# Kernel optimization log

Measured on AMD Instinct MI355X. Metric: run time of the kernel, lower is better.

Reference implementation:

```python
import jax, jax.numpy as jnp
import numpy as np

N, E = 50000, 800000
IN, HID, OUT = 128, 128, 64
BN_EPS = 1e-5


def _w(key, fan_in, fan_out):
    return jax.random.normal(key, (fan_in, fan_out), dtype=jnp.float32) / np.sqrt(fan_in)


def setup_inputs() -> dict:
    key = jax.random.key(0)
    ks = jax.random.split(key, 12)
    x = jax.random.normal(ks[0], (N, IN), dtype=jnp.float32)
    src = jax.random.randint(ks[1], (E,), 0, N, dtype=jnp.int32)
    dst = jax.random.randint(ks[2], (E,), 0, N, dtype=jnp.int32)
    eps = jax.random.normal(ks[3], (N, OUT), dtype=jnp.float32)
    return {
        "x": x, "src": src, "dst": dst, "eps": eps,
        # SAGEConv 1: in -> hidden (lin_l has bias, lin_r no bias, mean aggr)
        "W1l": _w(ks[4], IN, HID), "W1r": _w(ks[5], IN, HID), "b1": jnp.zeros((HID,), jnp.float32),
        "g1": jnp.ones((HID,), jnp.float32), "be1": jnp.zeros((HID,), jnp.float32),
        # SAGEConv 2: hidden -> 2*hidden
        "W2l": _w(ks[6], HID, 2 * HID), "W2r": _w(ks[7], HID, 2 * HID), "b2": jnp.zeros((2 * HID,), jnp.float32),
        "g2": jnp.ones((2 * HID,), jnp.float32), "be2": jnp.zeros((2 * HID,), jnp.float32),
        # SAGEConv 3: 2*hidden -> 2*out
        "W3l": _w(ks[8], 2 * HID, 2 * OUT), "W3r": _w(ks[9], 2 * HID, 2 * OUT), "b3": jnp.zeros((2 * OUT,), jnp.float32),
    }


def _sage(h, src, dst, Wl, Wr, b):
    # mean-aggregate source features at destination nodes, then two GEMMs
    msg = jax.ops.segment_sum(h[src], dst, num_segments=N)          # [N, F]
    deg = jax.ops.segment_sum(jnp.ones((src.shape[0],), h.dtype), dst, num_segments=N)
    aggr = msg / jnp.maximum(deg, 1.0)[:, None]
    return aggr @ Wl + h @ Wr + b


def _bn(h, gamma, beta):
    m = jnp.mean(h, axis=0)
    v = jnp.var(h, axis=0)
    return gamma * (h - m) * jax.lax.rsqrt(v + BN_EPS) + beta


def reference(x, src, dst, eps, W1l, W1r, b1, g1, be1, W2l, W2r, b2, g2, be2, W3l, W3r, b3):
    h = jax.nn.relu(_sage(x, src, dst, W1l, W1r, b1))
    h = _bn(h, g1, be1)                       # dropout = identity (eval)
    h = jax.nn.relu(_sage(h, src, dst, W2l, W2r, b2))
    h = _bn(h, g2, be2)
    h = _sage(h, src, dst, W3l, W3r, b3)      # [N, 2*OUT]
    mean, log_std = jnp.split(h, 2, axis=-1)
    z = mean + jnp.exp(log_std) * eps         # reparameterize
    return z
```

## Files before the change

kernel.cpp:

```cpp
#include <hip/hip_runtime.h>
#include <math.h>

#define N_NODES 50000
#define N_EDGES 800000
#define BN_EPS_F 1e-5f
#define SCAN_BS 512
#define SCAN_NB 98
#define GXP 392

typedef unsigned short ushort_t;
typedef unsigned int uint_t;
typedef __attribute__((ext_vector_type(8))) short bf16x8;
typedef __attribute__((ext_vector_type(4))) float f32x4;

static __device__ __forceinline__ float4 ld4(const float* p) {
    return *reinterpret_cast<const float4*>(p);
}
static __device__ __forceinline__ float bf2f(ushort_t u) {
    return __uint_as_float(((uint_t)u) << 16);
}
static __device__ __forceinline__ ushort_t f2b(float f) {
    uint_t u = __float_as_uint(f);
    u += 0x7fffu + ((u >> 16) & 1u);
    return (ushort_t)(u >> 16);
}
static __device__ __forceinline__ void gload16(const void* g, void* l) {
    __builtin_amdgcn_global_load_lds(
        (const __attribute__((address_space(1))) void*)g,
        (__attribute__((address_space(3))) void*)l, 16, 0, 0);
}


__global__ void k_zero_i32(int* __restrict__ p, int n) {
    int i = blockIdx.x * blockDim.x + threadIdx.x;
    if (i < n) p[i] = 0;
}

__global__ void k_countrank(const int* __restrict__ dst, int* __restrict__ deg,
                            int* __restrict__ rank) {
    int e = blockIdx.x * blockDim.x + threadIdx.x;
    if (e < N_EDGES) rank[e] = atomicAdd(&deg[dst[e]], 1);
}

__global__ void k_scan1(const int* __restrict__ deg, int* __restrict__ offs, int* __restrict__ bsum) {
    __shared__ int sh[SCAN_BS];
    int t = threadIdx.x;
    int g = blockIdx.x * SCAN_BS + t;
    int v = (g < N_NODES) ? deg[g] : 0;
    sh[t] = v;
    __syncthreads();
    for (int off = 1; off < SCAN_BS; off <<= 1) {
        int add = (t >= off) ? sh[t - off] : 0;
        __syncthreads();
        sh[t] += add;
        __syncthreads();
    }
    if (g < N_NODES) offs[g] = sh[t] - v;
    if (t == SCAN_BS - 1) bsum[blockIdx.x] = sh[t];
}

__global__ void k_scan2(int* __restrict__ bsum, int nb) {
    __shared__ int sh[128];
    int t = threadIdx.x;
    int v = (t < nb) ? bsum[t] : 0;
    sh[t] = v;
    __syncthreads();
    for (int off = 1; off < 128; off <<= 1) {
        int add = (t >= off) ? sh[t - off] : 0;
        __syncthreads();
        sh[t] += add;
        __syncthreads();
    }
    if (t < nb) bsum[t] = sh[t] - v;
}

__global__ void k_scan3(const int* __restrict__ deg, int* __restrict__ offs,
                        const int* __restrict__ bsum, float* __restrict__ inv_deg) {
    int g = blockIdx.x * blockDim.x + threadIdx.x;
    if (g < N_NODES) {
        offs[g] += bsum[g / SCAN_BS];
        int d = deg[g];
        inv_deg[g] = 1.0f / (float)(d > 1 ? d : 1);
    }
}

__global__ void k_fill2(const int* __restrict__ src, const int* __restrict__ dst,
                        const int* __restrict__ offs, const int* __restrict__ rank,
                        int* __restrict__ eids) {
    int e = blockIdx.x * blockDim.x + threadIdx.x;
    if (e < N_EDGES) eids[offs[dst[e]] + rank[e]] = src[e];
}


__global__ void k_f2b8(const float* __restrict__ in, ushort_t* __restrict__ out, int n8) {
    int i = blockIdx.x * blockDim.x + threadIdx.x;
    if (i >= n8) return;
    float4 a = ld4(in + (size_t)i * 8);
    float4 b = ld4(in + (size_t)i * 8 + 4);
    uint_t o0 = (uint_t)f2b(a.x) | ((uint_t)f2b(a.y) << 16);
    uint_t o1 = (uint_t)f2b(a.z) | ((uint_t)f2b(a.w) << 16);
    uint_t o2 = (uint_t)f2b(b.x) | ((uint_t)f2b(b.y) << 16);
    uint_t o3 = (uint_t)f2b(b.z) | ((uint_t)f2b(b.w) << 16);
    *reinterpret_cast<uint4*>(out + (size_t)i * 8) = make_uint4(o0, o1, o2, o3);
}

__global__ void k_prep1(const float* __restrict__ W1l, const float* __restrict__ W1r,
                        const float* __restrict__ W2l, ushort_t* __restrict__ wt1l,
                        ushort_t* __restrict__ wt1r, ushort_t* __restrict__ wt2l) {
    int idx = blockIdx.x * 256 + threadIdx.x;
    if (idx < 16384) {
        int f = idx >> 7, k = idx & 127;
        wt1l[idx] = f2b(W1l[(size_t)k * 128 + f]);
    } else if (idx < 32768) {
        int j = idx - 16384;
        int f = j >> 7, k = j & 127;
        wt1r[j] = f2b(W1r[(size_t)k * 128 + f]);
    } else {
        int j = idx - 32768;
        int f = j >> 7, k = j & 127;
        wt2l[j] = f2b(W2l[(size_t)k * 256 + f]);
    }
}

__global__ void k_prep2(const float* __restrict__ W2r, const float* __restrict__ b2,
                        const float* __restrict__ scsh1, ushort_t* __restrict__ wt2r,
                        float* __restrict__ bias2) {
    int bid = blockIdx.x;
    if (bid < 128) {
        int idx = bid * 256 + threadIdx.x;
        int f = idx >> 7, k = idx & 127;
        wt2r[idx] = f2b(scsh1[k] * W2r[(size_t)k * 256 + f]);
    } else {
        int f = threadIdx.x;
        float s = b2[f];
        for (int k = 0; k < 128; ++k) s += scsh1[128 + k] * W2r[(size_t)k * 256 + f];
        bias2[f] = s;
    }
}

__global__ void k_prep3(const float* __restrict__ W3l, const float* __restrict__ W3r,
                        const float* __restrict__ b3, const float* __restrict__ scsh2,
                        ushort_t* __restrict__ wt3l, ushort_t* __restrict__ wt3r,
                        float* __restrict__ bias3l, float* __restrict__ bias3r) {
    int bid = blockIdx.x;
    if (bid < 256) {
        int half = bid >> 7;
        int idx = (bid & 127) * 256 + threadIdx.x;
        int f = idx >> 8, k = idx & 255;
        const float* W = half ? W3r : W3l;
        ushort_t* WT = half ? wt3r : wt3l;
        WT[idx] = f2b(scsh2[k] * W[(size_t)k * 128 + f]);
    } else {
        int t = threadIdx.x;
        int f = t & 127;
        const float* W = (t < 128) ? W3l : W3r;
        float s = (t < 128) ? 0.f : b3[f];
        for (int k = 0; k < 256; ++k) s += scsh2[256 + k] * W[(size_t)k * 128 + f];
        float* out = (t < 128) ? bias3l : bias3r;
        out[f] = s;
    }
}


#define ACCUM8(a) do { \
    acc[0] += bf2f((ushort_t)(a).x); acc[1] += bf2f((ushort_t)((a).x >> 16)); \
    acc[2] += bf2f((ushort_t)(a).y); acc[3] += bf2f((ushort_t)((a).y >> 16)); \
    acc[4] += bf2f((ushort_t)(a).z); acc[5] += bf2f((ushort_t)((a).z >> 16)); \
    acc[6] += bf2f((ushort_t)(a).w); acc[7] += bf2f((ushort_t)((a).w >> 16)); } while (0)

static __device__ __forceinline__ void gather_rows(
        const ushort_t* __restrict__ h, const int* __restrict__ eids,
        int beg, int d, int g, size_t coff, float* acc) {
    int j = 0;
    for (; j + 32 <= d; j += 32) {
        int s[8];
#pragma unroll
        for (int k = 0; k < 8; ++k) s[k] = eids[beg + j + k * 4 + g];
        uint4 a[8];
#pragma unroll
        for (int k = 0; k < 8; ++k) a[k] = *reinterpret_cast<const uint4*>(h + (size_t)s[k] * 128 + coff);
#pragma unroll
        for (int k = 0; k < 8; ++k) ACCUM8(a[k]);
    }
    for (; j + 16 <= d; j += 16) {
        int s[4];
#pragma unroll
        for (int k = 0; k < 4; ++k) s[k] = eids[beg + j + k * 4 + g];
        uint4 a[4];
#pragma unroll
        for (int k = 0; k < 4; ++k) a[k] = *reinterpret_cast<const uint4*>(h + (size_t)s[k] * 128 + coff);
#pragma unroll
        for (int k = 0; k < 4; ++k) ACCUM8(a[k]);
    }
    for (; j + 8 <= d; j += 8) {
        int s0 = eids[beg + j + g];
        int s1 = eids[beg + j + 4 + g];
        uint4 a = *reinterpret_cast<const uint4*>(h + (size_t)s0 * 128 + coff);
        uint4 b = *reinterpret_cast<const uint4*>(h + (size_t)s1 * 128 + coff);
        ACCUM8(a); ACCUM8(b);
    }
    for (; j < d; j += 4) {
        int e = j + g;
        if (e < d) {
            int s0 = eids[beg + e];
            uint4 a = *reinterpret_cast<const uint4*>(h + (size_t)s0 * 128 + coff);
            ACCUM8(a);
        }
    }
}

template<int BN>
__global__ __launch_bounds__(256) void k_agg16(
        const ushort_t* __restrict__ h, const int* __restrict__ eids,
        const int* __restrict__ offs, const int* __restrict__ deg,
        const float* __restrict__ inv_deg, const float* __restrict__ scsh,
        ushort_t* __restrict__ out) {
    int node = (blockIdx.x * 256 + threadIdx.x) >> 6;
    int lane = threadIdx.x & 63;
    if (node >= N_NODES) return;
    const int g = lane >> 4;
    const int lr = lane & 15;
    float acc[8];
#pragma unroll
    for (int v = 0; v < 8; ++v) acc[v] = 0.f;
    const int beg = offs[node];
    const int d = deg[node];
    const size_t coff = (size_t)lr * 8;
    gather_rows(h, eids, beg, d, g, coff, acc);
#pragma unroll
    for (int v = 0; v < 8; ++v) acc[v] += __shfl_xor(acc[v], 16);
#pragma unroll
    for (int v = 0; v < 8; ++v) acc[v] += __shfl_xor(acc[v], 32);

    if (g == 0) {
        float sc = inv_deg[node];
        if (BN) {
            float4 sa0 = ld4(&scsh[lr * 8]), sa1 = ld4(&scsh[lr * 8 + 4]);
            float4 sb0 = ld4(&scsh[128 + lr * 8]), sb1 = ld4(&scsh[128 + lr * 8 + 4]);
            if (d > 0) {
                acc[0] = acc[0] * sc * sa0.x + sb0.x; acc[1] = acc[1] * sc * sa0.y + sb0.y;
                acc[2] = acc[2] * sc * sa0.z + sb0.z; acc[3] = acc[3] * sc * sa0.w + sb0.w;
                acc[4] = acc[4] * sc * sa1.x + sb1.x; acc[5] = acc[5] * sc * sa1.y + sb1.y;
                acc[6] = acc[6] * sc * sa1.z + sb1.z; acc[7] = acc[7] * sc * sa1.w + sb1.w;
            } else {
#pragma unroll
                for (int v = 0; v < 8; ++v) acc[v] = 0.f;
            }
        } else {
#pragma unroll
            for (int v = 0; v < 8; ++v) acc[v] *= sc;
        }
        uint4 o;
        o.x = (uint_t)f2b(acc[0]) | ((uint_t)f2b(acc[1]) << 16);
        o.y = (uint_t)f2b(acc[2]) | ((uint_t)f2b(acc[3]) << 16);
        o.z = (uint_t)f2b(acc[4]) | ((uint_t)f2b(acc[5]) << 16);
        o.w = (uint_t)f2b(acc[6]) | ((uint_t)f2b(acc[7]) << 16);
        *reinterpret_cast<uint4*>(out + (size_t)node * 128 + coff) = o;
    }
}

__global__ __launch_bounds__(256) void k_agg_reparam(
        const ushort_t* __restrict__ t3, const int* __restrict__ eids,
        const int* __restrict__ offs, const int* __restrict__ deg,
        const float* __restrict__ inv_deg, const float* __restrict__ u,
        const float* __restrict__ eps, float* __restrict__ z) {
    int node = (blockIdx.x * 256 + threadIdx.x) >> 6;
    int lane = threadIdx.x & 63;
    if (node >= N_NODES) return;
    const int g = lane >> 4;
    const int lr = lane & 15;
    float acc[8];
#pragma unroll
    for (int v = 0; v < 8; ++v) acc[v] = 0.f;
    const int beg = offs[node];
    const int d = deg[node];
    const size_t coff = (size_t)lr * 8;
    gather_rows(t3, eids, beg, d, g, coff, acc);
#pragma unroll
    for (int v = 0; v < 8; ++v) acc[v] += __shfl_xor(acc[v], 16);
#pragma unroll
    for (int v = 0; v < 8; ++v) acc[v] += __shfl_xor(acc[v], 32);
    float ls[8];
#pragma unroll
    for (int v = 0; v < 8; ++v) ls[v] = __shfl_down(acc[v], 8);

    if (g == 0 && lr < 8) {
        float sc = inv_deg[node];
        const float* um = u + (size_t)node * 128 + lr * 8;
        const float* ul = u + (size_t)node * 128 + 64 + lr * 8;
        const float* ep = eps + (size_t)node * 64 + lr * 8;
        float4 um0 = ld4(um), um1 = ld4(um + 4);
        float4 ul0 = ld4(ul), ul1 = ld4(ul + 4);
        float4 e0 = ld4(ep), e1 = ld4(ep + 4);
        float4 o0, o1;
        o0.x = (acc[0] * sc + um0.x) + expf(ls[0] * sc + ul0.x) * e0.x;
        o0.y = (acc[1] * sc + um0.y) + expf(ls[1] * sc + ul0.y) * e0.y;
        o0.z = (acc[2] * sc + um0.z) + expf(ls[2] * sc + ul0.z) * e0.z;
        o0.w = (acc[3] * sc + um0.w) + expf(ls[3] * sc + ul0.w) * e0.w;
        o1.x = (acc[4] * sc + um1.x) + expf(ls[4] * sc + ul1.x) * e1.x;
        o1.y = (acc[5] * sc + um1.y) + expf(ls[5] * sc + ul1.y) * e1.y;
        o1.z = (acc[6] * sc + um1.z) + expf(ls[6] * sc + ul1.z) * e1.z;
        o1.w = (acc[7] * sc + um1.w) + expf(ls[7] * sc + ul1.w) * e1.w;
        float* zp = z + (size_t)node * 64 + lr * 8;
        *reinterpret_cast<float4*>(zp) = o0;
        *reinterpret_cast<float4*>(zp + 4) = o1;
    }
}


template<int RELU, int OUTB, int DUAL, int BIAS, int STATS>
__global__ __launch_bounds__(256) void k_gemm_mfma(
        const ushort_t* __restrict__ A1, const ushort_t* __restrict__ A2,
        const ushort_t* __restrict__ B1, const ushort_t* __restrict__ B2,
        const float* __restrict__ bias, void* __restrict__ out,
        int K, int F, float* __restrict__ partials) {
    __shared__ __align__(16) short lds[8192];
    const int tid = threadIdx.x;
    const int lane = tid & 63;
    const int w = tid >> 6;
    const int row0 = blockIdx.x * 128;
    const int col0 = blockIdx.y * 128;
    const int wr = (w >> 1) * 64;
    const int wc = (w & 1) * 64;

    int rowA[2], slA[2];
#pragma unroll
    for (int p = 0; p < 2; ++p) {
        int c = (p * 4 + w) * 64 + lane;
        int r = c >> 2, sp = c & 3;
        rowA[p] = r;
        slA[p] = sp ^ ((r >> 1) & 3);
    }
    const int q = lane >> 4, lr = lane & 15;
    int aoff[4], boff[4];
#pragma unroll
    for (int f = 0; f < 4; ++f) {
        int ra = wr + f * 16 + lr;
        aoff[f] = ra * 32 + (q ^ ((ra >> 1) & 3)) * 8;
        int rb = wc + f * 16 + lr;
        boff[f] = 4096 + rb * 32 + (q ^ ((rb >> 1) & 3)) * 8;
    }

    f32x4 acc[4][4];
#pragma unroll
    for (int mf = 0; mf < 4; ++mf)
#pragma unroll
        for (int nf = 0; nf < 4; ++nf)
            acc[mf][nf] = (f32x4){0.f, 0.f, 0.f, 0.f};

    for (int m = 0; m < (DUAL ? 2 : 1); ++m) {
        const ushort_t* __restrict__ A = m ? A2 : A1;
        const ushort_t* __restrict__ B = m ? B2 : B1;
        for (int k0 = 0; k0 < K; k0 += 32) {
            __syncthreads();
#pragma unroll
            for (int p = 0; p < 2; ++p) {
                int gr = row0 + rowA[p];
                if (gr > N_NODES - 1) gr = N_NODES - 1;
                gload16(A + (size_t)gr * K + k0 + slA[p] * 8, &lds[(p * 4 + w) * 512]);
                int gc = col0 + rowA[p];
                gload16(B + (size_t)gc * K + k0 + slA[p] * 8, &lds[4096 + (p * 4 + w) * 512]);
            }
            asm volatile("s_waitcnt vmcnt(0)" ::: "memory");
            __syncthreads();
            bf16x8 av[4], bv[4];
#pragma unroll
            for (int f = 0; f < 4; ++f) {
                av[f] = *reinterpret_cast<const bf16x8*>(&lds[aoff[f]]);
                bv[f] = *reinterpret_cast<const bf16x8*>(&lds[boff[f]]);
            }
#pragma unroll
            for (int mf = 0; mf < 4; ++mf)
#pragma unroll
                for (int nf = 0; nf < 4; ++nf)
                    acc[mf][nf] = __builtin_amdgcn_mfma_f32_16x16x32_bf16(
                        av[mf], bv[nf], acc[mf][nf], 0, 0, 0);
        }
    }

    const int orow = row0 + wr + q * 4;
    const int ocol = col0 + wc + lr;
    float s[4], s2[4];
#pragma unroll
    for (int nf = 0; nf < 4; ++nf) { s[nf] = 0.f; s2[nf] = 0.f; }
#pragma unroll
    for (int nf = 0; nf < 4; ++nf) {
        int colg = ocol + nf * 16;
        float bvs = BIAS ? bias[colg] : 0.f;
#pragma unroll
        for (int mf = 0; mf < 4; ++mf) {
#pragma unroll
            for (int b = 0; b < 4; ++b) {
                int r = orow + mf * 16 + b;
                if (r < N_NODES) {
                    float v = acc[mf][nf][b] + bvs;
                    if (RELU) v = fmaxf(v, 0.f);
                    if (STATS) { s[nf] += v; s2[nf] += v * v; }
                    if (OUTB)
                        ((ushort_t*)out)[(size_t)r * F + colg] = f2b(v);
                    else
                        ((float*)out)[(size_t)r * F + colg] = v;
                }
            }
        }
    }

    if constexpr (STATS) {
        __syncthreads();
        float* sdf = (float*)lds;
        const int u = (w >> 1) * 4 + q;
#pragma unroll
        for (int nf = 0; nf < 4; ++nf) {
            int cb = wc + nf * 16 + lr;
            sdf[u * 128 + cb] = s[nf];
            sdf[1024 + u * 128 + cb] = s2[nf];
        }
        __syncthreads();
        if (tid < 128) {
            float ss = 0.f, qq = 0.f;
#pragma unroll
            for (int u2 = 0; u2 < 8; ++u2) {
                ss += sdf[u2 * 128 + tid];
                qq += sdf[1024 + u2 * 128 + tid];
            }
            int cg = col0 + tid;
            partials[(size_t)cg * GXP + blockIdx.x] = ss;
            partials[(size_t)(F + cg) * GXP + blockIdx.x] = qq;
        }
    }
}


template<int F>
__global__ __launch_bounds__(64) void k_bn_scsh(
        const float* __restrict__ partials, const float* __restrict__ gamma,
        const float* __restrict__ beta, float* __restrict__ scsh, int GX) {
    const int c = blockIdx.x;
    const int l = threadIdx.x;
    float s = 0.f, q2 = 0.f;
    for (int g = l; g < GX; g += 64) {
        s += partials[(size_t)c * GXP + g];
        q2 += partials[(size_t)(F + c) * GXP + g];
    }
#pragma unroll
    for (int off = 1; off < 64; off <<= 1) {
        s += __shfl_xor(s, off);
        q2 += __shfl_xor(q2, off);
    }
    if (l == 0) {
        float mean = s * (1.0f / N_NODES);
        float var = q2 * (1.0f / N_NODES) - mean * mean;
        float sc = gamma[c] * rsqrtf(var + BN_EPS_F);
        scsh[c] = sc;
        scsh[F + c] = beta[c] - mean * sc;
    }
}


extern "C" void kernel_launch(void* const* d_in, const int* in_sizes, int n_in,
                              void* d_out, int out_size, void* d_ws, size_t ws_size,
                              hipStream_t stream) {
    (void)in_sizes; (void)n_in; (void)out_size; (void)ws_size;
    const float* x   = (const float*)d_in[0];
    const int*   src = (const int*)d_in[1];
    const int*   dst = (const int*)d_in[2];
    const float* eps = (const float*)d_in[3];
    const float* W1l = (const float*)d_in[4];
    const float* W1r = (const float*)d_in[5];
    const float* b1  = (const float*)d_in[6];
    const float* g1  = (const float*)d_in[7];
    const float* be1 = (const float*)d_in[8];
    const float* W2l = (const float*)d_in[9];
    const float* W2r = (const float*)d_in[10];
    const float* b2  = (const float*)d_in[11];
    const float* g2  = (const float*)d_in[12];
    const float* be2 = (const float*)d_in[13];
    const float* W3l = (const float*)d_in[14];
    const float* W3r = (const float*)d_in[15];
    const float* b3  = (const float*)d_in[16];
    float* z = (float*)d_out;

    char* ws = (char*)d_ws;
    size_t off = 0;
    auto alloc = [&](size_t bytes) -> char* {
        char* p = ws + off;
        off += (bytes + 255) & ~(size_t)255;
        return p;
    };
    int*      deg    = (int*)alloc(N_NODES * 4);
    size_t zero_bytes = off;
    int*      rank   = (int*)alloc((size_t)N_EDGES * 4);
    float*    scshs  = (float*)alloc(1024 * 4);
    float*    biases = (float*)alloc(512 * 4);
    int*      offs   = (int*)alloc(N_NODES * 4);
    int*      bsum   = (int*)alloc(128 * 4);
    int*      eids   = (int*)alloc((size_t)N_EDGES * 4);
    float*    invd   = (float*)alloc(N_NODES * 4);
    ushort_t* xb     = (ushort_t*)alloc((size_t)N_NODES * 128 * 2);
    ushort_t* h1b    = (ushort_t*)alloc((size_t)N_NODES * 128 * 2);
    ushort_t* h2b    = (ushort_t*)alloc((size_t)N_NODES * 256 * 2);
    ushort_t* aggrb  = (ushort_t*)alloc((size_t)N_NODES * 256 * 2);
    float*    u3f    = (float*)alloc((size_t)N_NODES * 128 * 4);
    float*    parts  = (float*)alloc((size_t)512 * GXP * 4);
    ushort_t* wt1l   = (ushort_t*)alloc(128 * 128 * 2);
    ushort_t* wt1r   = (ushort_t*)alloc(128 * 128 * 2);
    ushort_t* wt2l   = (ushort_t*)alloc(256 * 128 * 2);
    ushort_t* wt2r   = (ushort_t*)alloc(256 * 128 * 2);
    ushort_t* wt3l   = (ushort_t*)alloc(128 * 256 * 2);
    ushort_t* wt3r   = (ushort_t*)alloc(128 * 256 * 2);
    ushort_t* t3b    = aggrb;

    float* scsh1  = scshs;
    float* scsh2  = scshs + 256;
    float* bias2  = biases;
    float* bias3l = biases + 256;
    float* bias3r = biases + 384;

    k_zero_i32<<<((int)(zero_bytes / 4) + 255) / 256, 256, 0, stream>>>((int*)ws, (int)(zero_bytes / 4));
    k_countrank<<<(N_EDGES + 255) / 256, 256, 0, stream>>>(dst, deg, rank);
    k_scan1<<<SCAN_NB, SCAN_BS, 0, stream>>>(deg, offs, bsum);
    k_scan2<<<1, 128, 0, stream>>>(bsum, SCAN_NB);
    k_scan3<<<(N_NODES + 255) / 256, 256, 0, stream>>>(deg, offs, bsum, invd);
    k_fill2<<<(N_EDGES + 255) / 256, 256, 0, stream>>>(src, dst, offs, rank, eids);

    k_f2b8<<<(N_NODES * 128 / 8 + 255) / 256, 256, 0, stream>>>(x, xb, N_NODES * 128 / 8);
    k_prep1<<<256, 256, 0, stream>>>(W1l, W1r, W2l, wt1l, wt1r, wt2l);

    const int AGG_BLKS = (N_NODES + 3) / 4;
    const int GX = (N_NODES + 127) / 128;

    k_agg16<0><<<AGG_BLKS, 256, 0, stream>>>(xb, eids, offs, deg, invd, nullptr, aggrb);
    k_gemm_mfma<1, 1, 1, 1, 1><<<dim3(GX, 1), 256, 0, stream>>>(aggrb, xb, wt1l, wt1r, b1, h1b, 128, 128, parts);
    k_bn_scsh<128><<<128, 64, 0, stream>>>(parts, g1, be1, scsh1, GX);

    k_prep2<<<129, 256, 0, stream>>>(W2r, b2, scsh1, wt2r, bias2);
    k_agg16<1><<<AGG_BLKS, 256, 0, stream>>>(h1b, eids, offs, deg, invd, scsh1, aggrb);
    k_gemm_mfma<1, 1, 1, 1, 1><<<dim3(GX, 2), 256, 0, stream>>>(aggrb, h1b, wt2l, wt2r, bias2, h2b, 128, 256, parts);
    k_bn_scsh<256><<<256, 64, 0, stream>>>(parts, g2, be2, scsh2, GX);

    k_prep3<<<257, 256, 0, stream>>>(W3l, W3r, b3, scsh2, wt3l, wt3r, bias3l, bias3r);
    k_gemm_mfma<0, 1, 0, 1, 0><<<dim3(GX, 1), 256, 0, stream>>>(h2b, nullptr, wt3l, nullptr, bias3l, t3b, 256, 128, nullptr);
    k_gemm_mfma<0, 0, 0, 1, 0><<<dim3(GX, 1), 256, 0, stream>>>(h2b, nullptr, wt3r, nullptr, bias3r, u3f, 256, 128, nullptr);
    k_agg_reparam<<<AGG_BLKS, 256, 0, stream>>>(t3b, eids, offs, deg, invd, u3f, eps, z);
}
```

Measured before the change: 299.5 us.

## Merge preprocessing kernels, use 16-bit edge indices, merge layer-3 GEMM launches

Edge degree counting, x-to-bf16 conversion and weight transposition now run as one launch, with blocks interleaved by role. The CSR rank and source-index arrays shrink from int32 to uint16, which halves their memory traffic in the fill and gather kernels. The two layer-3 GEMMs become one launch that uses blockIdx.y to pick the weight, bias and output format. The 16-bit indices rely on N < 65536 and on each per-node degree fitting in 16 bits.

New measurement: 269.9 us. 1.11x faster.

```diff
diff --git a/kernel.cpp b/kernel.cpp
--- a/kernel.cpp
+++ b/kernel.cpp
@@ -36,10 +36,42 @@
     if (i < n) p[i] = 0;
 }
 
-__global__ void k_countrank(const int* __restrict__ dst, int* __restrict__ deg,
-                            int* __restrict__ rank) {
-    int e = blockIdx.x * blockDim.x + threadIdx.x;
-    if (e < N_EDGES) rank[e] = atomicAdd(&deg[dst[e]], 1);
+__global__ void k_pre(const int* __restrict__ dst, int* __restrict__ deg,
+                      ushort_t* __restrict__ rank,
+                      const float* __restrict__ x, ushort_t* __restrict__ xb,
+                      const float* __restrict__ W1l, const float* __restrict__ W1r,
+                      const float* __restrict__ W2l, ushort_t* __restrict__ wt1l,
+                      ushort_t* __restrict__ wt1r, ushort_t* __restrict__ wt2l) {
+    int b = blockIdx.x;
+    if (b < 6250) {
+        int role = b & 1;
+        int id = (b >> 1) * 256 + threadIdx.x;
+        if (role == 0) {
+            rank[id] = (ushort_t)atomicAdd(&deg[dst[id]], 1);
+        } else {
+            float4 a = ld4(x + (size_t)id * 8);
+            float4 c = ld4(x + (size_t)id * 8 + 4);
+            uint_t o0 = (uint_t)f2b(a.x) | ((uint_t)f2b(a.y) << 16);
+            uint_t o1 = (uint_t)f2b(a.z) | ((uint_t)f2b(a.w) << 16);
+            uint_t o2 = (uint_t)f2b(c.x) | ((uint_t)f2b(c.y) << 16);
+            uint_t o3 = (uint_t)f2b(c.z) | ((uint_t)f2b(c.w) << 16);
+            *reinterpret_cast<uint4*>(xb + (size_t)id * 8) = make_uint4(o0, o1, o2, o3);
+        }
+    } else {
+        int idx = (b - 6250) * 256 + threadIdx.x;
+        if (idx < 16384) {
+            int f = idx >> 7, k = idx & 127;
+            wt1l[idx] = f2b(W1l[(size_t)k * 128 + f]);
+        } else if (idx < 32768) {
+            int j = idx - 16384;
+            int f = j >> 7, k = j & 127;
+            wt1r[j] = f2b(W1r[(size_t)k * 128 + f]);
+        } else {
+            int j = idx - 32768;
+            int f = j >> 7, k = j & 127;
+            wt2l[j] = f2b(W2l[(size_t)k * 256 + f]);
+        }
+    }
 }
 
 __global__ void k_scan1(const int* __restrict__ deg, int* __restrict__ offs, int* __restrict__ bsum) {
@@ -85,42 +117,12 @@
 }
 
 __global__ void k_fill2(const int* __restrict__ src, const int* __restrict__ dst,
-                        const int* __restrict__ offs, const int* __restrict__ rank,
-                        int* __restrict__ eids) {
+                        const int* __restrict__ offs, const ushort_t* __restrict__ rank,
+                        ushort_t* __restrict__ eids) {
     int e = blockIdx.x * blockDim.x + threadIdx.x;
-    if (e < N_EDGES) eids[offs[dst[e]] + rank[e]] = src[e];
-}
-
-
-__global__ void k_f2b8(const float* __restrict__ in, ushort_t* __restrict__ out, int n8) {
-    int i = blockIdx.x * blockDim.x + threadIdx.x;
-    if (i >= n8) return;
-    float4 a = ld4(in + (size_t)i * 8);
-    float4 b = ld4(in + (size_t)i * 8 + 4);
-    uint_t o0 = (uint_t)f2b(a.x) | ((uint_t)f2b(a.y) << 16);
-    uint_t o1 = (uint_t)f2b(a.z) | ((uint_t)f2b(a.w) << 16);
-    uint_t o2 = (uint_t)f2b(b.x) | ((uint_t)f2b(b.y) << 16);
-    uint_t o3 = (uint_t)f2b(b.z) | ((uint_t)f2b(b.w) << 16);
-    *reinterpret_cast<uint4*>(out + (size_t)i * 8) = make_uint4(o0, o1, o2, o3);
-}
-
-__global__ void k_prep1(const float* __restrict__ W1l, const float* __restrict__ W1r,
-                        const float* __restrict__ W2l, ushort_t* __restrict__ wt1l,
-                        ushort_t* __restrict__ wt1r, ushort_t* __restrict__ wt2l) {
-    int idx = blockIdx.x * 256 + threadIdx.x;
-    if (idx < 16384) {
-        int f = idx >> 7, k = idx & 127;
-        wt1l[idx] = f2b(W1l[(size_t)k * 128 + f]);
-    } else if (idx < 32768) {
-        int j = idx - 16384;
-        int f = j >> 7, k = j & 127;
-        wt1r[j] = f2b(W1r[(size_t)k * 128 + f]);
-    } else {
-        int j = idx - 32768;
-        int f = j >> 7, k = j & 127;
-        wt2l[j] = f2b(W2l[(size_t)k * 256 + f]);
-    }
-}
+    if (e < N_EDGES) eids[offs[dst[e]] + (int)rank[e]] = (ushort_t)src[e];
+}
+
 
 __global__ void k_prep2(const float* __restrict__ W2r, const float* __restrict__ b2,
                         const float* __restrict__ scsh1, ushort_t* __restrict__ wt2r,
@@ -169,7 +171,7 @@
     acc[6] += bf2f((ushort_t)(a).w); acc[7] += bf2f((ushort_t)((a).w >> 16)); } while (0)
 
 static __device__ __forceinline__ void gather_rows(
-        const ushort_t* __restrict__ h, const int* __restrict__ eids,
+        const ushort_t* __restrict__ h, const ushort_t* __restrict__ eids,
         int beg, int d, int g, size_t coff, float* acc) {
     int j = 0;
     for (; j + 32 <= d; j += 32) {
@@ -211,7 +213,7 @@
 
 template<int BN>
 __global__ __launch_bounds__(256) void k_agg16(
-        const ushort_t* __restrict__ h, const int* __restrict__ eids,
+        const ushort_t* __restrict__ h, const ushort_t* __restrict__ eids,
         const int* __restrict__ offs, const int* __restrict__ deg,
         const float* __restrict__ inv_deg, const float* __restrict__ scsh,
         ushort_t* __restrict__ out) {
@@ -260,7 +262,7 @@
 }
 
 __global__ __launch_bounds__(256) void k_agg_reparam(
-        const ushort_t* __restrict__ t3, const int* __restrict__ eids,
+        const ushort_t* __restrict__ t3, const ushort_t* __restrict__ eids,
         const int* __restrict__ offs, const int* __restrict__ deg,
         const float* __restrict__ inv_deg, const float* __restrict__ u,
         const float* __restrict__ eps, float* __restrict__ z) {
@@ -308,20 +310,26 @@
 }
 
 
-template<int RELU, int OUTB, int DUAL, int BIAS, int STATS>
+template<int RELU, int OUTB, int DUAL, int BIAS, int STATS, int SELY>
 __global__ __launch_bounds__(256) void k_gemm_mfma(
         const ushort_t* __restrict__ A1, const ushort_t* __restrict__ A2,
         const ushort_t* __restrict__ B1, const ushort_t* __restrict__ B2,
         const float* __restrict__ bias, void* __restrict__ out,
-        int K, int F, float* __restrict__ partials) {
+        int K, int F, float* __restrict__ partials,
+        const float* __restrict__ bias2, void* __restrict__ out2) {
     __shared__ __align__(16) short lds[8192];
     const int tid = threadIdx.x;
     const int lane = tid & 63;
     const int w = tid >> 6;
     const int row0 = blockIdx.x * 128;
-    const int col0 = blockIdx.y * 128;
+    const int col0 = SELY ? 0 : blockIdx.y * 128;
     const int wr = (w >> 1) * 64;
     const int wc = (w & 1) * 64;
+
+    const ushort_t* __restrict__ B0 = (SELY && blockIdx.y) ? B2 : B1;
+    const float* __restrict__ biasp = (SELY && blockIdx.y) ? bias2 : bias;
+    void* __restrict__ outp = (SELY && blockIdx.y) ? out2 : out;
+    const bool outb = SELY ? (blockIdx.y == 0) : (OUTB != 0);
 
     int rowA[2], slA[2];
 #pragma unroll
@@ -350,7 +358,7 @@
 
     for (int m = 0; m < (DUAL ? 2 : 1); ++m) {
         const ushort_t* __restrict__ A = m ? A2 : A1;
-        const ushort_t* __restrict__ B = m ? B2 : B1;
+        const ushort_t* __restrict__ B = m ? B2 : B0;
         for (int k0 = 0; k0 < K; k0 += 32) {
             __syncthreads();
 #pragma unroll
@@ -386,7 +394,7 @@
 #pragma unroll
     for (int nf = 0; nf < 4; ++nf) {
         int colg = ocol + nf * 16;
-        float bvs = BIAS ? bias[colg] : 0.f;
+        float bvs = BIAS ? biasp[colg] : 0.f;
 #pragma unroll
         for (int mf = 0; mf < 4; ++mf) {
 #pragma unroll
@@ -396,10 +404,10 @@
                     float v = acc[mf][nf][b] + bvs;
                     if (RELU) v = fmaxf(v, 0.f);
                     if (STATS) { s[nf] += v; s2[nf] += v * v; }
-                    if (OUTB)
-                        ((ushort_t*)out)[(size_t)r * F + colg] = f2b(v);
+                    if (outb)
+                        ((ushort_t*)outp)[(size_t)r * F + colg] = f2b(v);
                     else
-                        ((float*)out)[(size_t)r * F + colg] = v;
+                        ((float*)outp)[(size_t)r * F + colg] = v;
                 }
             }
         }
@@ -489,12 +497,12 @@
     };
     int*      deg    = (int*)alloc(N_NODES * 4);
     size_t zero_bytes = off;
-    int*      rank   = (int*)alloc((size_t)N_EDGES * 4);
+    ushort_t* rank   = (ushort_t*)alloc((size_t)N_EDGES * 2);
+    ushort_t* eids   = (ushort_t*)alloc((size_t)N_EDGES * 2);
     float*    scshs  = (float*)alloc(1024 * 4);
     float*    biases = (float*)alloc(512 * 4);
     int*      offs   = (int*)alloc(N_NODES * 4);
     int*      bsum   = (int*)alloc(128 * 4);
-    int*      eids   = (int*)alloc((size_t)N_EDGES * 4);
     float*    invd   = (float*)alloc(N_NODES * 4);
     ushort_t* xb     = (ushort_t*)alloc((size_t)N_NODES * 128 * 2);
     ushort_t* h1b    = (ushort_t*)alloc((size_t)N_NODES * 128 * 2);
@@ -517,29 +525,25 @@
     float* bias3r = biases + 384;
 
     k_zero_i32<<<((int)(zero_bytes / 4) + 255) / 256, 256, 0, stream>>>((int*)ws, (int)(zero_bytes / 4));
-    k_countrank<<<(N_EDGES + 255) / 256, 256, 0, stream>>>(dst, deg, rank);
+    k_pre<<<6506, 256, 0, stream>>>(dst, deg, rank, x, xb, W1l, W1r, W2l, wt1l, wt1r, wt2l);
     k_scan1<<<SCAN_NB, SCAN_BS, 0, stream>>>(deg, offs, bsum);
     k_scan2<<<1, 128, 0, stream>>>(bsum, SCAN_NB);
     k_scan3<<<(N_NODES + 255) / 256, 256, 0, stream>>>(deg, offs, bsum, invd);
     k_fill2<<<(N_EDGES + 255) / 256, 256, 0, stream>>>(src, dst, offs, rank, eids);
 
-    k_f2b8<<<(N_NODES * 128 / 8 + 255) / 256, 256, 0, stream>>>(x, xb, N_NODES * 128 / 8);
-    k_prep1<<<256, 256, 0, stream>>>(W1l, W1r, W2l, wt1l, wt1r, wt2l);
-
     const int AGG_BLKS = (N_NODES + 3) / 4;
     const int GX = (N_NODES + 127) / 128;
 
     k_agg16<0><<<AGG_BLKS, 256, 0, stream>>>(xb, eids, offs, deg, invd, nullptr, aggrb);
-    k_gemm_mfma<1, 1, 1, 1, 1><<<dim3(GX, 1), 256, 0, stream>>>(aggrb, xb, wt1l, wt1r, b1, h1b, 128, 128, parts);
+    k_gemm_mfma<1, 1, 1, 1, 1, 0><<<dim3(GX, 1), 256, 0, stream>>>(aggrb, xb, wt1l, wt1r, b1, h1b, 128, 128, parts, nullptr, nullptr);
     k_bn_scsh<128><<<128, 64, 0, stream>>>(parts, g1, be1, scsh1, GX);
 
     k_prep2<<<129, 256, 0, stream>>>(W2r, b2, scsh1, wt2r, bias2);
     k_agg16<1><<<AGG_BLKS, 256, 0, stream>>>(h1b, eids, offs, deg, invd, scsh1, aggrb);
-    k_gemm_mfma<1, 1, 1, 1, 1><<<dim3(GX, 2), 256, 0, stream>>>(aggrb, h1b, wt2l, wt2r, bias2, h2b, 128, 256, parts);
+    k_gemm_mfma<1, 1, 1, 1, 1, 0><<<dim3(GX, 2), 256, 0, stream>>>(aggrb, h1b, wt2l, wt2r, bias2, h2b, 128, 256, parts, nullptr, nullptr);
     k_bn_scsh<256><<<256, 64, 0, stream>>>(parts, g2, be2, scsh2, GX);
 
     k_prep3<<<257, 256, 0, stream>>>(W3l, W3r, b3, scsh2, wt3l, wt3r, bias3l, bias3r);
-    k_gemm_mfma<0, 1, 0, 1, 0><<<dim3(GX, 1), 256, 0, stream>>>(h2b, nullptr, wt3l, nullptr, bias3l, t3b, 256, 128, nullptr);
-    k_gemm_mfma<0, 0, 0, 1, 0><<<dim3(GX, 1), 256, 0, stream>>>(h2b, nullptr, wt3r, nullptr, bias3r, u3f, 256, 128, nullptr);
+    k_gemm_mfma<0, 1, 0, 1, 0, 1><<<dim3(GX, 2), 256, 0, stream>>>(h2b, nullptr, wt3l, wt3r, bias3l, t3b, 256, 128, nullptr, bias3r, u3f);
     k_agg_reparam<<<AGG_BLKS, 256, 0, stream>>>(t3b, eids, offs, deg, invd, u3f, eps, z);
 }
```
